# Performance work log

Measured on AMD Instinct MI355X. Metric: run time of the kernel, lower is better.

Reference implementation:

```python
import jax, jax.numpy as jnp
import numpy as np

N = 40000      # nodes
E = 640000     # edges
R = 4          # relations (n_edge_features)
F = 128        # n_node_features
H = 128        # n_hidden
NB = 2         # num_convolution_blocks
G = 64         # graphs in batch
OUT = 10       # n_output
MAXDEG = 10    # PyG MFConv default max_degree


def setup_inputs() -> dict:
    key = jax.random.key(0)
    ks = jax.random.split(key, 20)
    s = 0.05
    return {
        "x": jax.random.normal(ks[0], (N, F), dtype=jnp.float32),
        "edge_index": jax.random.randint(ks[1], (2, E), 0, N, dtype=jnp.int32),
        "edge_attr": jax.random.randint(ks[2], (E,), 0, R, dtype=jnp.int32),
        "batch_idx": jnp.sort(jax.random.randint(ks[3], (N,), 0, G, dtype=jnp.int32)),
        # node embedding Linear(F -> H)
        "W0": jax.random.normal(ks[4], (F, H), dtype=jnp.float32) * s,
        "b0": jnp.zeros((H,), dtype=jnp.float32),
        # per-block RGCNConv params (stacked over blocks)
        "rgcn_Wrel": jax.random.normal(ks[5], (NB, R, H, H), dtype=jnp.float32) * s,
        "rgcn_Wroot": jax.random.normal(ks[6], (NB, H, H), dtype=jnp.float32) * s,
        "rgcn_b": jnp.zeros((NB, H), dtype=jnp.float32),
        # per-block MFConv params: lins_l (bias) and lins_r (no bias), one per degree 0..MAXDEG
        "mf_Wl": jax.random.normal(ks[7], (NB, MAXDEG + 1, H, H), dtype=jnp.float32) * s,
        "mf_bl": jnp.zeros((NB, MAXDEG + 1, H), dtype=jnp.float32),
        "mf_Wr": jax.random.normal(ks[8], (NB, MAXDEG + 1, H, H), dtype=jnp.float32) * s,
        # after-pool MLP
        "W1": jax.random.normal(ks[9], (H, H), dtype=jnp.float32) * s,
        "b1": jnp.zeros((H,), dtype=jnp.float32),
        "W2": jax.random.normal(ks[10], (H, OUT), dtype=jnp.float32) * s,
        "b2": jnp.zeros((OUT,), dtype=jnp.float32),
    }


def _rgcn(h, Wrel, Wroot, b, src, dst, etype):
    # PyG RGCNConv: per-relation mean of neighbor features, then relation GEMM, plus root + bias
    n = h.shape[0]
    idx = dst * R + etype                                   # fused (node, relation) segment id
    msg = h[src]                                            # [E, H] gather
    sums = jax.ops.segment_sum(msg, idx, num_segments=n * R).reshape(n, R, -1)
    cnt = jax.ops.segment_sum(jnp.ones((msg.shape[0],), h.dtype), idx,
                              num_segments=n * R).reshape(n, R, 1)
    mean = jnp.where(cnt > 0, sums / jnp.maximum(cnt, 1.0), 0.0)
    return jnp.einsum('nrh,rho->no', mean, Wrel) + h @ Wroot + b


def _mfconv(h, Wl, bl, Wr, src, dst, deg):
    # PyG MFConv: sum-aggregate neighbors, then degree-specific lin_l(agg) + lin_r(x)
    n = h.shape[0]
    agg = jax.ops.segment_sum(h[src], dst, num_segments=n)  # [N, H]
    out = jnp.zeros((n, Wl.shape[-1]), h.dtype)
    for d in range(MAXDEG + 1):                             # small fixed loop over degree buckets
        m = (deg == d).astype(h.dtype)[:, None]
        out = out + m * (agg @ Wl[d] + bl[d] + h @ Wr[d])
    return out


def reference(x, edge_index, edge_attr, batch_idx,
              W0, b0, rgcn_Wrel, rgcn_Wroot, rgcn_b,
              mf_Wl, mf_bl, mf_Wr, W1, b1, W2, b2):
    src, dst = edge_index[0], edge_index[1]
    etype = edge_attr
    n = x.shape[0]
    # node degree at targets (all relations), clamped to MAXDEG (PyG MFConv)
    deg = jnp.clip(jax.ops.segment_sum(jnp.ones((src.shape[0],), jnp.int32), dst,
                                       num_segments=n), 0, MAXDEG)
    h = x @ W0 + b0
    for blk in range(NB):
        h = jax.nn.relu(h)
        h = _rgcn(h, rgcn_Wrel[blk], rgcn_Wroot[blk], rgcn_b[blk], src, dst, etype)
        h = jax.nn.relu(h)
        h = _mfconv(h, mf_Wl[blk], mf_bl[blk], mf_Wr[blk], src, dst, deg)
    pooled = jax.ops.segment_sum(h, batch_idx, num_segments=G)  # global add pool [G, H]
    out = jax.nn.relu(pooled @ W1 + b1) @ W2 + b2
    return out
```

## Files before the change

### kernel.cpp

```cpp
#include <hip/hip_runtime.h>
#include <hip/hip_bf16.h>

#define N_NODES 40000
#define N_EDGES 640000
#define R_REL 4
#define F_IN 128
#define H_DIM 128
#define NBLK 2
#define G_GRAPHS 64
#define N_OUT 10
#define MAXDEG 10
#define NSCAN_BLK ((N_NODES + 255) / 256)

typedef unsigned short u16;
typedef float f32x4 __attribute__((ext_vector_type(4)));
typedef short bf16x8 __attribute__((ext_vector_type(8)));

__device__ __forceinline__ float relu_f(float x){ return x > 0.f ? x : 0.f; }

__device__ __forceinline__ u16 f2bf(float f){
  union { float f; unsigned int u; } v; v.f = f;
  unsigned int r = v.u + 0x7fffu + ((v.u >> 16) & 1u);
  return (u16)(r >> 16);
}
__device__ __forceinline__ float b2f(u16 u){
  union { unsigned int u; float f; } v; v.u = ((unsigned int)u) << 16; return v.f;
}
__device__ __forceinline__ float blo(unsigned v){ return b2f((u16)v); }
__device__ __forceinline__ float bhi(unsigned v){ return b2f((u16)(v >> 16)); }

__device__ __forceinline__ void gload16(const void* g, void* l){
  __builtin_amdgcn_global_load_lds(
      (const __attribute__((address_space(1))) void*)g,
      (__attribute__((address_space(3))) void*)l, 16, 0, 0);
}

__global__ void k_cnt(const int* __restrict__ dst, const int* __restrict__ et, int* __restrict__ cnt4){
  int e = blockIdx.x * blockDim.x + threadIdx.x;
  if (e >= N_EDGES) return;
  atomicAdd(&cnt4[dst[e] * R_REL + et[e]], 1);
}

__global__ __launch_bounds__(256) void k_scan_a(const int* __restrict__ cnt4, int* __restrict__ deg,
                                                int* __restrict__ row_ptr, int* __restrict__ bsum,
                                                int* __restrict__ bhist){
  __shared__ int s[256];
  __shared__ int lh[16];
  int tid = threadIdx.x;
  int i = blockIdx.x * 256 + tid;
  if (tid < 16) lh[tid] = 0;
  int d = 0;
  if (i < N_NODES){
    int4 c = *(const int4*)(cnt4 + (size_t)i * 4);
    d = c.x + c.y + c.z + c.w;
    deg[i] = d;
  }
  s[tid] = d;
  __syncthreads();
  if (i < N_NODES){
    int dc = d > MAXDEG ? MAXDEG : d;
    atomicAdd(&lh[dc], 1);
  }
  for (int o = 1; o < 256; o <<= 1){
    int t = (tid >= o) ? s[tid - o] : 0;
    __syncthreads();
    s[tid] += t;
    __syncthreads();
  }
  if (i < N_NODES) row_ptr[i] = s[tid] - d;
  if (tid == 255) bsum[blockIdx.x] = s[255];
  if (tid <= MAXDEG) bhist[blockIdx.x * (MAXDEG + 1) + tid] = lh[tid];
}

__global__ __launch_bounds__(256) void k_scan_b(int* __restrict__ bsum, int* __restrict__ bbase){
  __shared__ int s[256];
  int tid = threadIdx.x;
  int v = (tid < NSCAN_BLK) ? bsum[tid] : 0;
  s[tid] = v;
  __syncthreads();
  for (int o = 1; o < 256; o <<= 1){
    int t = (tid >= o) ? s[tid - o] : 0;
    __syncthreads();
    s[tid] += t;
    __syncthreads();
  }
  if (tid < NSCAN_BLK) bbase[tid] = s[tid] - v;
}

__global__ __launch_bounds__(256) void k_scan_c(int* __restrict__ row_ptr, const int* __restrict__ bbase,
                                                const int* __restrict__ cnt4, int* __restrict__ rel_off){
  int i = blockIdx.x * 256 + threadIdx.x;
  if (i < N_NODES){
    int base = row_ptr[i] + bbase[blockIdx.x];
    row_ptr[i] = base;
    int4 c = *(const int4*)(cnt4 + (size_t)i * 4);
    int4 o;
    o.x = base;
    o.y = base + c.x;
    o.z = o.y + c.y;
    o.w = o.z + c.z;
    *(int4*)(rel_off + (size_t)i * 4) = o;
  }
  if (i == 0) row_ptr[N_NODES] = N_EDGES;
}

__global__ void k_csr_fill(const int* __restrict__ src, const int* __restrict__ dst,
                           const int* __restrict__ et, const int* __restrict__ rel_off,
                           int* __restrict__ cursor, int* __restrict__ esrc){
  int e = blockIdx.x * blockDim.x + threadIdx.x;
  if (e >= N_EDGES) return;
  int cell = dst[e] * R_REL + et[e];
  int p = atomicAdd(&cursor[cell], 1);
  esrc[rel_off[cell] + p] = src[e];
}

__global__ __launch_bounds__(64) void k_bscan(const int* __restrict__ bhist, int* __restrict__ pbase,
                                              int* __restrict__ bcount, int* __restrict__ boff){
  __shared__ int cnt_s[MAXDEG + 1];
  __shared__ int off_s[MAXDEG + 1];
  int d = threadIdx.x;
  if (d <= MAXDEG){
    int run = 0;
    for (int b = 0; b < NSCAN_BLK; ++b){
      pbase[b * (MAXDEG + 1) + d] = run;
      run += bhist[b * (MAXDEG + 1) + d];
    }
    cnt_s[d] = run;
    bcount[d] = run;
  }
  __syncthreads();
  if (d == 0){
    int s = 0;
    for (int dd = 0; dd <= MAXDEG; ++dd){ off_s[dd] = s; boff[dd] = s; s += cnt_s[dd]; }
  }
  __syncthreads();
  if (d <= MAXDEG){
    int base = off_s[d];
    for (int b = 0; b < NSCAN_BLK; ++b) pbase[b * (MAXDEG + 1) + d] += base;
  }
}

__global__ __launch_bounds__(256) void k_bfill(const int* __restrict__ deg, const int* __restrict__ pbase,
                                               int* __restrict__ perm){
  __shared__ int lh[MAXDEG + 1];
  int tid = threadIdx.x;
  if (tid <= MAXDEG) lh[tid] = 0;
  __syncthreads();
  int i = blockIdx.x * 256 + tid;
  if (i < N_NODES){
    int d = deg[i]; if (d > MAXDEG) d = MAXDEG;
    int lpos = atomicAdd(&lh[d], 1);
    perm[pbase[blockIdx.x * (MAXDEG + 1) + d] + lpos] = i;
  }
}

__global__ __launch_bounds__(256) void k_cvtW_all(const float* __restrict__ s0, const float* __restrict__ s1,
                                                  const float* __restrict__ s2, const float* __restrict__ s3,
                                                  const float* __restrict__ s4,
                                                  u16* __restrict__ d0, u16* __restrict__ d1,
                                                  u16* __restrict__ d2, u16* __restrict__ d3,
                                                  u16* __restrict__ d4){
  __shared__ float s[32][33];
  int b = blockIdx.x;
  int m = b >> 4, tile = b & 15;
  const float* S; u16* D; int base;
  if (m < 1){ S = s0; D = d0; base = m; }
  else if (m < 9){ S = s1; D = d1; base = m - 1; }
  else if (m < 11){ S = s2; D = d2; base = m - 9; }
  else if (m < 33){ S = s3; D = d3; base = m - 11; }
  else { S = s4; D = d4; base = m - 33; }
  S += (size_t)base * 16384;
  D += (size_t)base * 16384;
  int tr = (tile >> 2) * 32, tc = (tile & 3) * 32;
  int c = threadIdx.x & 31, r0 = threadIdx.x >> 5;
  #pragma unroll
  for (int i = 0; i < 4; ++i){
    int r = r0 + i * 8;
    s[r][c] = S[(size_t)(tr + r) * 128 + tc + c];
  }
  __syncthreads();
  #pragma unroll
  for (int i = 0; i < 4; ++i){
    int r = r0 + i * 8;
    D[(size_t)(tc + r) * 128 + tr + c] = f2bf(s[c][r]);
  }
}

__global__ void k_cvtx(const float* __restrict__ x, u16* __restrict__ xb){
  int t = blockIdx.x * 256 + threadIdx.x;
  if (t >= (N_NODES * H_DIM) / 4) return;
  float4 v = ((const float4*)x)[t];
  uint2 o = make_uint2((unsigned)f2bf(v.x) | ((unsigned)f2bf(v.y) << 16),
                       (unsigned)f2bf(v.z) | ((unsigned)f2bf(v.w) << 16));
  ((uint2*)xb)[t] = o;
}

__global__ __launch_bounds__(256) void k_rgcn_agg(const u16* __restrict__ hb,
                                                  const int* __restrict__ rel_off,
                                                  const int* __restrict__ row_ptr,
                                                  const int* __restrict__ esrc,
                                                  u16* __restrict__ meanb){
  int node = blockIdx.x * 4 + (threadIdx.x >> 6);
  int lane = threadIdx.x & 63;
  int4 ro = *(const int4*)(rel_off + (size_t)node * 4);
  int nend = row_ptr[node + 1];
  int begs[5] = {ro.x, ro.y, ro.z, ro.w, nend};
  #pragma unroll
  for (int r = 0; r < R_REL; ++r){
    int beg = begs[r], end = begs[r + 1];
    float a0 = 0.f, a1 = 0.f;
    int e = beg;
    for (; e + 4 <= end; e += 4){
      int s0 = esrc[e], s1 = esrc[e + 1], s2 = esrc[e + 2], s3 = esrc[e + 3];
      unsigned v0 = *(const unsigned*)(hb + (size_t)s0 * H_DIM + lane * 2);
      unsigned v1 = *(const unsigned*)(hb + (size_t)s1 * H_DIM + lane * 2);
      unsigned v2 = *(const unsigned*)(hb + (size_t)s2 * H_DIM + lane * 2);
      unsigned v3 = *(const unsigned*)(hb + (size_t)s3 * H_DIM + lane * 2);
      a0 += blo(v0) + blo(v1) + blo(v2) + blo(v3);
      a1 += bhi(v0) + bhi(v1) + bhi(v2) + bhi(v3);
    }
    for (; e < end; ++e){
      unsigned v = *(const unsigned*)(hb + (size_t)esrc[e] * H_DIM + lane * 2);
      a0 += blo(v); a1 += bhi(v);
    }
    int c = end - beg;
    float inv = c > 0 ? 1.f / (float)c : 0.f;
    unsigned o = (unsigned)f2bf(a0 * inv) | ((unsigned)f2bf(a1 * inv) << 16);
    *(unsigned*)(meanb + ((size_t)node * R_REL + r) * H_DIM + lane * 2) = o;
  }
}

__global__ __launch_bounds__(256) void k_mf_agg(const u16* __restrict__ hb,
                                                const int* __restrict__ row_ptr,
                                                const int* __restrict__ esrc,
                                                u16* __restrict__ aggb){
  int node = blockIdx.x * 4 + (threadIdx.x >> 6);
  int lane = threadIdx.x & 63;
  int beg = row_ptr[node], end = row_ptr[node + 1];
  float a0 = 0.f, a1 = 0.f;
  int e = beg;
  for (; e + 4 <= end; e += 4){
    int s0 = esrc[e], s1 = esrc[e + 1], s2 = esrc[e + 2], s3 = esrc[e + 3];
    unsigned v0 = *(const unsigned*)(hb + (size_t)s0 * H_DIM + lane * 2);
    unsigned v1 = *(const unsigned*)(hb + (size_t)s1 * H_DIM + lane * 2);
    unsigned v2 = *(const unsigned*)(hb + (size_t)s2 * H_DIM + lane * 2);
    unsigned v3 = *(const unsigned*)(hb + (size_t)s3 * H_DIM + lane * 2);
    a0 += blo(v0) + blo(v1) + blo(v2) + blo(v3);
    a1 += bhi(v0) + bhi(v1) + bhi(v2) + bhi(v3);
  }
  for (; e < end; ++e){
    unsigned v = *(const unsigned*)(hb + (size_t)esrc[e] * H_DIM + lane * 2);
    a0 += blo(v); a1 += bhi(v);
  }
  unsigned o = (unsigned)f2bf(a0) | ((unsigned)f2bf(a1) << 16);
  *(unsigned*)(aggb + (size_t)node * H_DIM + lane * 2) = o;
}


__global__ __launch_bounds__(512) void k_gemm0(const u16* __restrict__ xb, const u16* __restrict__ wt,
                                               const float* __restrict__ bias, u16* __restrict__ hbo){
  __shared__ u16 lds[32][128];
  int tid = threadIdx.x;
  int w = tid >> 6, lane = tid & 63;
  int m0 = blockIdx.x * 32;
  int rg = lane >> 4, cb = (lane & 15) << 4;
  int srow = w * 4 + rg;
  int swcb = cb ^ ((srow & 7) << 4);
  gload16(xb + (size_t)(m0 + srow) * F_IN + (swcb >> 1), &lds[w * 4][0]);
  __syncthreads();

  int arow = lane & 15, kg = lane >> 4;
  int col = w * 16 + arow;
  f32x4 acc[2];
  acc[0] = (f32x4){0.f, 0.f, 0.f, 0.f};
  acc[1] = (f32x4){0.f, 0.f, 0.f, 0.f};
  bf16x8 b[4];
  #pragma unroll
  for (int kk = 0; kk < 4; ++kk)
    b[kk] = *(const bf16x8*)(wt + (size_t)col * F_IN + kk * 32 + kg * 8);
  #pragma unroll
  for (int rt = 0; rt < 2; ++rt){
    int row = rt * 16 + arow;
    const char* base = (const char*)&lds[0][0] + row * 256;
    int sx = (row & 7) << 4;
    #pragma unroll
    for (int kk = 0; kk < 4; ++kk){
      bf16x8 a = *(const bf16x8*)(base + ((kk * 64 + kg * 16) ^ sx));
      acc[rt] = __builtin_amdgcn_mfma_f32_16x16x32_bf16(a, b[kk], acc[rt], 0, 0, 0);
    }
  }
  float bb = bias[col];
  #pragma unroll
  for (int rt = 0; rt < 2; ++rt)
    #pragma unroll
    for (int j = 0; j < 4; ++j){
      int gr = m0 + rt * 16 + kg * 4 + j;
      hbo[(size_t)gr * H_DIM + col] = f2bf(relu_f(acc[rt][j] + bb));
    }
}

__global__ __launch_bounds__(512) void k_rgcn_gemm(const u16* __restrict__ meanb, const u16* __restrict__ hb,
                                                   const u16* __restrict__ wrel, const u16* __restrict__ wroot,
                                                   const float* __restrict__ bias, u16* __restrict__ hbo){
  __shared__ u16 lds[5][32][128];
  int tid = threadIdx.x;
  int w = tid >> 6, lane = tid & 63;
  int m0 = blockIdx.x * 32;
  int rg = lane >> 4, cb = (lane & 15) << 4;
  int srow = w * 4 + rg;
  int swcb = cb ^ ((srow & 7) << 4);
  #pragma unroll
  for (int s = 0; s < 4; ++s)
    gload16(meanb + ((size_t)(m0 + srow) * R_REL + s) * H_DIM + (swcb >> 1), &lds[s][w * 4][0]);
  gload16(hb + (size_t)(m0 + srow) * H_DIM + (swcb >> 1), &lds[4][w * 4][0]);
  __syncthreads();

  int arow = lane & 15, kg = lane >> 4;
  int col = w * 16 + arow;
  f32x4 acc[2];
  acc[0] = (f32x4){0.f, 0.f, 0.f, 0.f};
  acc[1] = (f32x4){0.f, 0.f, 0.f, 0.f};
  #pragma unroll
  for (int s = 0; s < 5; ++s){
    const u16* WT = (s < 4) ? wrel + (size_t)s * 16384 : wroot;
    bf16x8 b[4];
    #pragma unroll
    for (int kk = 0; kk < 4; ++kk)
      b[kk] = *(const bf16x8*)(WT + (size_t)col * H_DIM + kk * 32 + kg * 8);
    #pragma unroll
    for (int rt = 0; rt < 2; ++rt){
      int row = rt * 16 + arow;
      const char* base = (const char*)&lds[s][0][0] + row * 256;
      int sx = (row & 7) << 4;
      #pragma unroll
      for (int kk = 0; kk < 4; ++kk){
        bf16x8 a = *(const bf16x8*)(base + ((kk * 64 + kg * 16) ^ sx));
        acc[rt] = __builtin_amdgcn_mfma_f32_16x16x32_bf16(a, b[kk], acc[rt], 0, 0, 0);
      }
    }
  }
  float bb = bias[col];
  #pragma unroll
  for (int rt = 0; rt < 2; ++rt)
    #pragma unroll
    for (int j = 0; j < 4; ++j){
      int gr = m0 + rt * 16 + kg * 4 + j;
      hbo[(size_t)gr * H_DIM + col] = f2bf(relu_f(acc[rt][j] + bb));
    }
}

template<int FINAL>
__global__ __launch_bounds__(512) void k_mf_gemm(const u16* __restrict__ aggb, const u16* __restrict__ hb,
                                                 const u16* __restrict__ wl, const u16* __restrict__ wr,
                                                 const float* __restrict__ bl,
                                                 const int* __restrict__ bcount, const int* __restrict__ boff,
                                                 const int* __restrict__ perm,
                                                 u16* __restrict__ hbo, float* __restrict__ hf){
  __shared__ u16 lds[2][32][128];
  __shared__ int rows_s[32];
  int t = blockIdx.x;
  int d = -1, tile = 0;
  for (int dd = 0; dd <= MAXDEG; ++dd){
    int nt = (bcount[dd] + 31) >> 5;
    if (t < nt){ d = dd; tile = t; break; }
    t -= nt;
  }
  if (d < 0) return;
  int cnt_d = bcount[d];
  int start = boff[d] + tile * 32;
  int nrows = cnt_d - tile * 32; if (nrows > 32) nrows = 32;

  int tid = threadIdx.x;
  int w = tid >> 6, lane = tid & 63;
  if (tid < 32) rows_s[tid] = (tid < nrows) ? perm[start + tid] : -1;

  int rg = lane >> 4, cb = (lane & 15) << 4;
  int srow = w * 4 + rg;
  int swcb = cb ^ ((srow & 7) << 4);
  int node = perm[start + (srow < nrows ? srow : 0)];
  gload16(aggb + (size_t)node * H_DIM + (swcb >> 1), &lds[0][w * 4][0]);
  gload16(hb   + (size_t)node * H_DIM + (swcb >> 1), &lds[1][w * 4][0]);
  __syncthreads();

  int arow = lane & 15, kg = lane >> 4;
  int col = w * 16 + arow;
  f32x4 acc[2];
  acc[0] = (f32x4){0.f, 0.f, 0.f, 0.f};
  acc[1] = (f32x4){0.f, 0.f, 0.f, 0.f};
  #pragma unroll
  for (int s = 0; s < 2; ++s){
    const u16* WT = (s ? wr : wl) + (size_t)d * 16384;
    bf16x8 b[4];
    #pragma unroll
    for (int kk = 0; kk < 4; ++kk)
      b[kk] = *(const bf16x8*)(WT + (size_t)col * H_DIM + kk * 32 + kg * 8);
    #pragma unroll
    for (int rt = 0; rt < 2; ++rt){
      int row = rt * 16 + arow;
      const char* base = (const char*)&lds[s][0][0] + row * 256;
      int sx = (row & 7) << 4;
      #pragma unroll
      for (int kk = 0; kk < 4; ++kk){
        bf16x8 a = *(const bf16x8*)(base + ((kk * 64 + kg * 16) ^ sx));
        acc[rt] = __builtin_amdgcn_mfma_f32_16x16x32_bf16(a, b[kk], acc[rt], 0, 0, 0);
      }
    }
  }
  float bb = bl[(size_t)d * H_DIM + col];
  #pragma unroll
  for (int rt = 0; rt < 2; ++rt)
    #pragma unroll
    for (int j = 0; j < 4; ++j){
      int gr = rows_s[rt * 16 + kg * 4 + j];
      if (gr >= 0){
        float v = acc[rt][j] + bb;
        if (FINAL) hf[(size_t)gr * H_DIM + col] = v;
        else       hbo[(size_t)gr * H_DIM + col] = f2bf(relu_f(v));
      }
    }
}

__global__ void k_goff(const int* __restrict__ batch, int* __restrict__ goff){
  int n = blockIdx.x * blockDim.x + threadIdx.x;
  if (n >= N_NODES) return;
  int b = batch[n];
  int bp = (n == 0) ? -1 : batch[n - 1];
  for (int g = bp + 1; g <= b; ++g) goff[g] = n;
  if (n == N_NODES - 1){
    for (int g = b + 1; g <= G_GRAPHS; ++g) goff[g] = N_NODES;
  }
}

__global__ __launch_bounds__(256) void k_pool(const float* __restrict__ h, const int* __restrict__ goff,
                                              float* __restrict__ pooled){
  __shared__ float4 sred[8][32];
  int g = blockIdx.x;
  int tid = threadIdx.x;
  int rg = tid >> 5, lane = tid & 31;
  int beg = goff[g], end = goff[g + 1];
  float4 acc = make_float4(0.f, 0.f, 0.f, 0.f);
  for (int n = beg + rg; n < end; n += 8){
    float4 v = ((const float4*)(h + (size_t)n * H_DIM))[lane];
    acc.x += v.x; acc.y += v.y; acc.z += v.z; acc.w += v.w;
  }
  sred[rg][lane] = acc;
  __syncthreads();
  if (tid < 32){
    float4 s = sred[0][tid];
    #pragma unroll
    for (int r = 1; r < 8; ++r){
      float4 v = sred[r][tid];
      s.x += v.x; s.y += v.y; s.z += v.z; s.w += v.w;
    }
    *(float4*)(pooled + (size_t)g * H_DIM + tid * 4) = s;
  }
}

__global__ void k_mlp1(const float* __restrict__ pooled, const float* __restrict__ W1,
                       const float* __restrict__ b1, float* __restrict__ T){
  int t = blockIdx.x * blockDim.x + threadIdx.x;
  if (t >= G_GRAPHS * H_DIM) return;
  int n = t >> 7, j = t & 127;
  float s = b1[j];
  for (int k = 0; k < H_DIM; ++k) s += pooled[n * H_DIM + k] * W1[k * H_DIM + j];
  T[t] = relu_f(s);
}

__global__ void k_mlp2(const float* __restrict__ T, const float* __restrict__ W2,
                       const float* __restrict__ b2, float* __restrict__ out){
  int t = blockIdx.x * blockDim.x + threadIdx.x;
  if (t >= G_GRAPHS * N_OUT) return;
  int n = t / N_OUT, j = t - n * N_OUT;
  float s = b2[j];
  for (int k = 0; k < H_DIM; ++k) s += T[n * H_DIM + k] * W2[k * N_OUT + j];
  out[t] = s;
}

extern "C" void kernel_launch(void* const* d_in, const int* in_sizes, int n_in,
                              void* d_out, int out_size, void* d_ws, size_t ws_size,
                              hipStream_t stream){
  const float* x      = (const float*)d_in[0];
  const int*   ei     = (const int*)d_in[1];
  const int*   ea     = (const int*)d_in[2];
  const int*   batch  = (const int*)d_in[3];
  const float* W0     = (const float*)d_in[4];
  const float* b0     = (const float*)d_in[5];
  const float* rWrel  = (const float*)d_in[6];
  const float* rWroot = (const float*)d_in[7];
  const float* rb     = (const float*)d_in[8];
  const float* mWl    = (const float*)d_in[9];
  const float* mbl    = (const float*)d_in[10];
  const float* mWr    = (const float*)d_in[11];
  const float* W1     = (const float*)d_in[12];
  const float* b1     = (const float*)d_in[13];
  const float* W2     = (const float*)d_in[14];
  const float* b2     = (const float*)d_in[15];
  float* out = (float*)d_out;

  const int* src = ei;
  const int* dst = ei + N_EDGES;

  char* ws = (char*)d_ws;
  size_t off = 0;
  auto alloc = [&](size_t bytes) -> void* {
    void* p = ws + off;
    off += (bytes + 255) & ~(size_t)255;
    return p;
  };
  u16* xb      = (u16*)alloc((size_t)N_NODES * H_DIM * 2);
  u16* hbA     = (u16*)alloc((size_t)N_NODES * H_DIM * 2);
  u16* hbB     = (u16*)alloc((size_t)N_NODES * H_DIM * 2);
  u16* meanb   = (u16*)alloc((size_t)N_NODES * R_REL * H_DIM * 2);
  u16* aggb    = meanb;
  float* hf    = (float*)alloc((size_t)N_NODES * H_DIM * 4);
  u16* wt0     = (u16*)alloc((size_t)1 * 16384 * 2);
  u16* wtRel   = (u16*)alloc((size_t)NBLK * R_REL * 16384 * 2);
  u16* wtRoot  = (u16*)alloc((size_t)NBLK * 16384 * 2);
  u16* wtWl    = (u16*)alloc((size_t)NBLK * (MAXDEG + 1) * 16384 * 2);
  u16* wtWr    = (u16*)alloc((size_t)NBLK * (MAXDEG + 1) * 16384 * 2);
  float* pooled = (float*)alloc((size_t)G_GRAPHS * H_DIM * 4);
  float* T      = (float*)alloc((size_t)G_GRAPHS * H_DIM * 4);
  int* cnt4     = (int*)alloc((size_t)N_NODES * R_REL * 4);
  int* deg      = (int*)alloc((size_t)N_NODES * 4);
  int* row_ptr  = (int*)alloc((size_t)(N_NODES + 1) * 4);
  int* rel_off  = (int*)alloc((size_t)N_NODES * R_REL * 4);
  int* cursor   = (int*)alloc((size_t)N_NODES * R_REL * 4);
  int* esrc     = (int*)alloc((size_t)N_EDGES * 4);
  int* bsum     = (int*)alloc((size_t)NSCAN_BLK * 4);
  int* bbase    = (int*)alloc((size_t)NSCAN_BLK * 4);
  int* bhist    = (int*)alloc((size_t)NSCAN_BLK * (MAXDEG + 1) * 4);
  int* pbase    = (int*)alloc((size_t)NSCAN_BLK * (MAXDEG + 1) * 4);
  int* perm     = (int*)alloc((size_t)N_NODES * 4);
  int* bcount   = (int*)alloc(16 * 4);
  int* boff     = (int*)alloc(16 * 4);
  int* goff     = (int*)alloc((size_t)(G_GRAPHS + 1) * 4);

  hipMemsetAsync(cnt4, 0, (size_t)N_NODES * R_REL * 4, stream);
  hipMemsetAsync(cursor, 0, (size_t)N_NODES * R_REL * 4, stream);

  k_cnt<<<(N_EDGES + 255) / 256, 256, 0, stream>>>(dst, ea, cnt4);
  k_scan_a<<<NSCAN_BLK, 256, 0, stream>>>(cnt4, deg, row_ptr, bsum, bhist);
  k_scan_b<<<1, 256, 0, stream>>>(bsum, bbase);
  k_scan_c<<<NSCAN_BLK, 256, 0, stream>>>(row_ptr, bbase, cnt4, rel_off);
  k_csr_fill<<<(N_EDGES + 255) / 256, 256, 0, stream>>>(src, dst, ea, rel_off, cursor, esrc);
  k_bscan<<<1, 64, 0, stream>>>(bhist, pbase, bcount, boff);
  k_bfill<<<NSCAN_BLK, 256, 0, stream>>>(deg, pbase, perm);
  k_goff<<<(N_NODES + 255) / 256, 256, 0, stream>>>(batch, goff);

  k_cvtW_all<<<55 * 16, 256, 0, stream>>>(W0, rWrel, rWroot, mWl, mWr,
                                          wt0, wtRel, wtRoot, wtWl, wtWr);
  k_cvtx<<<(N_NODES * H_DIM / 4 + 255) / 256, 256, 0, stream>>>(x, xb);

  k_gemm0<<<N_NODES / 32, 512, 0, stream>>>(xb, wt0, b0, hbA);

  u16* hin = hbA;
  u16* hout = hbB;
  for (int blk = 0; blk < NBLK; ++blk){
    k_rgcn_agg<<<N_NODES / 4, 256, 0, stream>>>(hin, rel_off, row_ptr, esrc, meanb);
    k_rgcn_gemm<<<N_NODES / 32, 512, 0, stream>>>(meanb, hin,
        wtRel + (size_t)blk * R_REL * 16384,
        wtRoot + (size_t)blk * 16384,
        rb + (size_t)blk * H_DIM, hout);
    { u16* tmp = hin; hin = hout; hout = tmp; }

    k_mf_agg<<<N_NODES / 4, 256, 0, stream>>>(hin, row_ptr, esrc, aggb);
    const u16* wl_b = wtWl + (size_t)blk * (MAXDEG + 1) * 16384;
    const u16* wr_b = wtWr + (size_t)blk * (MAXDEG + 1) * 16384;
    const float* bl_b = mbl + (size_t)blk * (MAXDEG + 1) * H_DIM;
    int grid_mf = N_NODES / 32 + MAXDEG + 1;
    if (blk == NBLK - 1)
      k_mf_gemm<1><<<grid_mf, 512, 0, stream>>>(aggb, hin, wl_b, wr_b, bl_b,
                                                bcount, boff, perm, hout, hf);
    else
      k_mf_gemm<0><<<grid_mf, 512, 0, stream>>>(aggb, hin, wl_b, wr_b, bl_b,
                                                bcount, boff, perm, hout, hf);
    { u16* tmp = hin; hin = hout; hout = tmp; }
  }

  k_pool<<<G_GRAPHS, 256, 0, stream>>>(hf, goff, pooled);
  k_mlp1<<<(G_GRAPHS * H_DIM + 255) / 256, 256, 0, stream>>>(pooled, W1, b1, T);
  k_mlp2<<<(G_GRAPHS * N_OUT + 255) / 256, 256, 0, stream>>>(T, W2, b2, out);
}
```

Baseline: 400.5 us.

## Fuse neighbor aggregation into RGCN and MFConv GEMM kernels via LDS staging

Removes the separate RGCN and MFConv aggregation kernels. Each GEMM block now gathers and averages or sums its own 32 rows' neighbor features and writes the bf16 results straight into swizzled LDS, so the intermediate meanb/aggb buffers are never written to or read from global memory. CSR fill also seeds the per-cell cursor with the relation offsets in scan_c, which drops a memset and an indirect load. The cost is that gather latency now sits inside the GEMM blocks, each wave serially handles 4 rows, and there are fewer waves in flight than with the 4-nodes-per-256-thread aggregation grids.

```diff
diff --git a/kernel.cpp b/kernel.cpp
--- a/kernel.cpp
+++ b/kernel.cpp
@@ -88,7 +88,8 @@
 }
 
 __global__ __launch_bounds__(256) void k_scan_c(int* __restrict__ row_ptr, const int* __restrict__ bbase,
-                                                const int* __restrict__ cnt4, int* __restrict__ rel_off){
+                                                const int* __restrict__ cnt4, int* __restrict__ rel_off,
+                                                int* __restrict__ cursor){
   int i = blockIdx.x * 256 + threadIdx.x;
   if (i < N_NODES){
     int base = row_ptr[i] + bbase[blockIdx.x];
@@ -100,18 +101,19 @@
     o.z = o.y + c.y;
     o.w = o.z + c.z;
     *(int4*)(rel_off + (size_t)i * 4) = o;
+    *(int4*)(cursor + (size_t)i * 4) = o;
   }
   if (i == 0) row_ptr[N_NODES] = N_EDGES;
 }
 
 __global__ void k_csr_fill(const int* __restrict__ src, const int* __restrict__ dst,
-                           const int* __restrict__ et, const int* __restrict__ rel_off,
+                           const int* __restrict__ et,
                            int* __restrict__ cursor, int* __restrict__ esrc){
   int e = blockIdx.x * blockDim.x + threadIdx.x;
   if (e >= N_EDGES) return;
   int cell = dst[e] * R_REL + et[e];
   int p = atomicAdd(&cursor[cell], 1);
-  esrc[rel_off[cell] + p] = src[e];
+  esrc[p] = src[e];
 }
 
 __global__ __launch_bounds__(64) void k_bscan(const int* __restrict__ bhist, int* __restrict__ pbase,
@@ -195,67 +197,6 @@
   ((uint2*)xb)[t] = o;
 }
 
-__global__ __launch_bounds__(256) void k_rgcn_agg(const u16* __restrict__ hb,
-                                                  const int* __restrict__ rel_off,
-                                                  const int* __restrict__ row_ptr,
-                                                  const int* __restrict__ esrc,
-                                                  u16* __restrict__ meanb){
-  int node = blockIdx.x * 4 + (threadIdx.x >> 6);
-  int lane = threadIdx.x & 63;
-  int4 ro = *(const int4*)(rel_off + (size_t)node * 4);
-  int nend = row_ptr[node + 1];
-  int begs[5] = {ro.x, ro.y, ro.z, ro.w, nend};
-  #pragma unroll
-  for (int r = 0; r < R_REL; ++r){
-    int beg = begs[r], end = begs[r + 1];
-    float a0 = 0.f, a1 = 0.f;
-    int e = beg;
-    for (; e + 4 <= end; e += 4){
-      int s0 = esrc[e], s1 = esrc[e + 1], s2 = esrc[e + 2], s3 = esrc[e + 3];
-      unsigned v0 = *(const unsigned*)(hb + (size_t)s0 * H_DIM + lane * 2);
-      unsigned v1 = *(const unsigned*)(hb + (size_t)s1 * H_DIM + lane * 2);
-      unsigned v2 = *(const unsigned*)(hb + (size_t)s2 * H_DIM + lane * 2);
-      unsigned v3 = *(const unsigned*)(hb + (size_t)s3 * H_DIM + lane * 2);
-      a0 += blo(v0) + blo(v1) + blo(v2) + blo(v3);
-      a1 += bhi(v0) + bhi(v1) + bhi(v2) + bhi(v3);
-    }
-    for (; e < end; ++e){
-      unsigned v = *(const unsigned*)(hb + (size_t)esrc[e] * H_DIM + lane * 2);
-      a0 += blo(v); a1 += bhi(v);
-    }
-    int c = end - beg;
-    float inv = c > 0 ? 1.f / (float)c : 0.f;
-    unsigned o = (unsigned)f2bf(a0 * inv) | ((unsigned)f2bf(a1 * inv) << 16);
-    *(unsigned*)(meanb + ((size_t)node * R_REL + r) * H_DIM + lane * 2) = o;
-  }
-}
-
-__global__ __launch_bounds__(256) void k_mf_agg(const u16* __restrict__ hb,
-                                                const int* __restrict__ row_ptr,
-                                                const int* __restrict__ esrc,
-                                                u16* __restrict__ aggb){
-  int node = blockIdx.x * 4 + (threadIdx.x >> 6);
-  int lane = threadIdx.x & 63;
-  int beg = row_ptr[node], end = row_ptr[node + 1];
-  float a0 = 0.f, a1 = 0.f;
-  int e = beg;
-  for (; e + 4 <= end; e += 4){
-    int s0 = esrc[e], s1 = esrc[e + 1], s2 = esrc[e + 2], s3 = esrc[e + 3];
-    unsigned v0 = *(const unsigned*)(hb + (size_t)s0 * H_DIM + lane * 2);
-    unsigned v1 = *(const unsigned*)(hb + (size_t)s1 * H_DIM + lane * 2);
-    unsigned v2 = *(const unsigned*)(hb + (size_t)s2 * H_DIM + lane * 2);
-    unsigned v3 = *(const unsigned*)(hb + (size_t)s3 * H_DIM + lane * 2);
-    a0 += blo(v0) + blo(v1) + blo(v2) + blo(v3);
-    a1 += bhi(v0) + bhi(v1) + bhi(v2) + bhi(v3);
-  }
-  for (; e < end; ++e){
-    unsigned v = *(const unsigned*)(hb + (size_t)esrc[e] * H_DIM + lane * 2);
-    a0 += blo(v); a1 += bhi(v);
-  }
-  unsigned o = (unsigned)f2bf(a0) | ((unsigned)f2bf(a1) << 16);
-  *(unsigned*)(aggb + (size_t)node * H_DIM + lane * 2) = o;
-}
-
 
 __global__ __launch_bounds__(512) void k_gemm0(const u16* __restrict__ xb, const u16* __restrict__ wt,
                                                const float* __restrict__ bias, u16* __restrict__ hbo){
@@ -299,20 +240,55 @@
     }
 }
 
-__global__ __launch_bounds__(512) void k_rgcn_gemm(const u16* __restrict__ meanb, const u16* __restrict__ hb,
-                                                   const u16* __restrict__ wrel, const u16* __restrict__ wroot,
-                                                   const float* __restrict__ bias, u16* __restrict__ hbo){
+__global__ __launch_bounds__(512) void k_rgcn_fused(const u16* __restrict__ hb,
+                                                    const int* __restrict__ rel_off,
+                                                    const int* __restrict__ row_ptr,
+                                                    const int* __restrict__ esrc,
+                                                    const u16* __restrict__ wrel, const u16* __restrict__ wroot,
+                                                    const float* __restrict__ bias, u16* __restrict__ hbo){
   __shared__ u16 lds[5][32][128];
   int tid = threadIdx.x;
   int w = tid >> 6, lane = tid & 63;
   int m0 = blockIdx.x * 32;
-  int rg = lane >> 4, cb = (lane & 15) << 4;
-  int srow = w * 4 + rg;
-  int swcb = cb ^ ((srow & 7) << 4);
-  #pragma unroll
-  for (int s = 0; s < 4; ++s)
-    gload16(meanb + ((size_t)(m0 + srow) * R_REL + s) * H_DIM + (swcb >> 1), &lds[s][w * 4][0]);
-  gload16(hb + (size_t)(m0 + srow) * H_DIM + (swcb >> 1), &lds[4][w * 4][0]);
+  {
+    int rg = lane >> 4, cb = (lane & 15) << 4;
+    int srow = w * 4 + rg;
+    int swcb = cb ^ ((srow & 7) << 4);
+    gload16(hb + (size_t)(m0 + srow) * H_DIM + (swcb >> 1), &lds[4][w * 4][0]);
+  }
+  #pragma unroll
+  for (int i = 0; i < 4; ++i){
+    int row = w * 4 + i;
+    int node = m0 + row;
+    int4 ro = *(const int4*)(rel_off + (size_t)node * 4);
+    int nend = row_ptr[node + 1];
+    int begs[5] = {ro.x, ro.y, ro.z, ro.w, nend};
+    int sx = (row & 7) << 4;
+    char* ldsb = (char*)&lds[0][0][0];
+    #pragma unroll
+    for (int r = 0; r < R_REL; ++r){
+      int beg = begs[r], end = begs[r + 1];
+      float a0 = 0.f, a1 = 0.f;
+      int e = beg;
+      for (; e + 4 <= end; e += 4){
+        int s0 = esrc[e], s1 = esrc[e + 1], s2 = esrc[e + 2], s3 = esrc[e + 3];
+        unsigned v0 = *(const unsigned*)(hb + (size_t)s0 * H_DIM + lane * 2);
+        unsigned v1 = *(const unsigned*)(hb + (size_t)s1 * H_DIM + lane * 2);
+        unsigned v2 = *(const unsigned*)(hb + (size_t)s2 * H_DIM + lane * 2);
+        unsigned v3 = *(const unsigned*)(hb + (size_t)s3 * H_DIM + lane * 2);
+        a0 += blo(v0) + blo(v1) + blo(v2) + blo(v3);
+        a1 += bhi(v0) + bhi(v1) + bhi(v2) + bhi(v3);
+      }
+      for (; e < end; ++e){
+        unsigned v = *(const unsigned*)(hb + (size_t)esrc[e] * H_DIM + lane * 2);
+        a0 += blo(v); a1 += bhi(v);
+      }
+      int c = end - beg;
+      float inv = c > 0 ? 1.f / (float)c : 0.f;
+      unsigned o = (unsigned)f2bf(a0 * inv) | ((unsigned)f2bf(a1 * inv) << 16);
+      *(unsigned*)(ldsb + (size_t)r * 8192 + row * 256 + ((lane * 4) ^ sx)) = o;
+    }
+  }
   __syncthreads();
 
   int arow = lane & 15, kg = lane >> 4;
@@ -350,12 +326,14 @@
 }
 
 template<int FINAL>
-__global__ __launch_bounds__(512) void k_mf_gemm(const u16* __restrict__ aggb, const u16* __restrict__ hb,
-                                                 const u16* __restrict__ wl, const u16* __restrict__ wr,
-                                                 const float* __restrict__ bl,
-                                                 const int* __restrict__ bcount, const int* __restrict__ boff,
-                                                 const int* __restrict__ perm,
-                                                 u16* __restrict__ hbo, float* __restrict__ hf){
+__global__ __launch_bounds__(512) void k_mf_fused(const u16* __restrict__ hb,
+                                                  const int* __restrict__ row_ptr,
+                                                  const int* __restrict__ esrc,
+                                                  const u16* __restrict__ wl, const u16* __restrict__ wr,
+                                                  const float* __restrict__ bl,
+                                                  const int* __restrict__ bcount, const int* __restrict__ boff,
+                                                  const int* __restrict__ perm,
+                                                  u16* __restrict__ hbo, float* __restrict__ hf){
   __shared__ u16 lds[2][32][128];
   __shared__ int rows_s[32];
   int t = blockIdx.x;
@@ -374,12 +352,39 @@
   int w = tid >> 6, lane = tid & 63;
   if (tid < 32) rows_s[tid] = (tid < nrows) ? perm[start + tid] : -1;
 
-  int rg = lane >> 4, cb = (lane & 15) << 4;
-  int srow = w * 4 + rg;
-  int swcb = cb ^ ((srow & 7) << 4);
-  int node = perm[start + (srow < nrows ? srow : 0)];
-  gload16(aggb + (size_t)node * H_DIM + (swcb >> 1), &lds[0][w * 4][0]);
-  gload16(hb   + (size_t)node * H_DIM + (swcb >> 1), &lds[1][w * 4][0]);
+  {
+    int rg = lane >> 4, cb = (lane & 15) << 4;
+    int srow = w * 4 + rg;
+    int swcb = cb ^ ((srow & 7) << 4);
+    int node = perm[start + (srow < nrows ? srow : 0)];
+    gload16(hb + (size_t)node * H_DIM + (swcb >> 1), &lds[1][w * 4][0]);
+  }
+  #pragma unroll
+  for (int i = 0; i < 4; ++i){
+    int row = w * 4 + i;
+    if (row < nrows){
+      int node = perm[start + row];
+      int beg = row_ptr[node], end = row_ptr[node + 1];
+      float a0 = 0.f, a1 = 0.f;
+      int e = beg;
+      for (; e + 4 <= end; e += 4){
+        int s0 = esrc[e], s1 = esrc[e + 1], s2 = esrc[e + 2], s3 = esrc[e + 3];
+        unsigned v0 = *(const unsigned*)(hb + (size_t)s0 * H_DIM + lane * 2);
+        unsigned v1 = *(const unsigned*)(hb + (size_t)s1 * H_DIM + lane * 2);
+        unsigned v2 = *(const unsigned*)(hb + (size_t)s2 * H_DIM + lane * 2);
+        unsigned v3 = *(const unsigned*)(hb + (size_t)s3 * H_DIM + lane * 2);
+        a0 += blo(v0) + blo(v1) + blo(v2) + blo(v3);
+        a1 += bhi(v0) + bhi(v1) + bhi(v2) + bhi(v3);
+      }
+      for (; e < end; ++e){
+        unsigned v = *(const unsigned*)(hb + (size_t)esrc[e] * H_DIM + lane * 2);
+        a0 += blo(v); a1 += bhi(v);
+      }
+      unsigned o = (unsigned)f2bf(a0) | ((unsigned)f2bf(a1) << 16);
+      int sx = (row & 7) << 4;
+      *(unsigned*)((char*)&lds[0][0][0] + row * 256 + ((lane * 4) ^ sx)) = o;
+    }
+  }
   __syncthreads();
 
   int arow = lane & 15, kg = lane >> 4;
@@ -510,8 +515,6 @@
   u16* xb      = (u16*)alloc((size_t)N_NODES * H_DIM * 2);
   u16* hbA     = (u16*)alloc((size_t)N_NODES * H_DIM * 2);
   u16* hbB     = (u16*)alloc((size_t)N_NODES * H_DIM * 2);
-  u16* meanb   = (u16*)alloc((size_t)N_NODES * R_REL * H_DIM * 2);
-  u16* aggb    = meanb;
   float* hf    = (float*)alloc((size_t)N_NODES * H_DIM * 4);
   u16* wt0     = (u16*)alloc((size_t)1 * 16384 * 2);
   u16* wtRel   = (u16*)alloc((size_t)NBLK * R_REL * 16384 * 2);
@@ -536,13 +539,12 @@
   int* goff     = (int*)alloc((size_t)(G_GRAPHS + 1) * 4);
 
   hipMemsetAsync(cnt4, 0, (size_t)N_NODES * R_REL * 4, stream);
-  hipMemsetAsync(cursor, 0, (size_t)N_NODES * R_REL * 4, stream);
 
   k_cnt<<<(N_EDGES + 255) / 256, 256, 0, stream>>>(dst, ea, cnt4);
   k_scan_a<<<NSCAN_BLK, 256, 0, stream>>>(cnt4, deg, row_ptr, bsum, bhist);
   k_scan_b<<<1, 256, 0, stream>>>(bsum, bbase);
-  k_scan_c<<<NSCAN_BLK, 256, 0, stream>>>(row_ptr, bbase, cnt4, rel_off);
-  k_csr_fill<<<(N_EDGES + 255) / 256, 256, 0, stream>>>(src, dst, ea, rel_off, cursor, esrc);
+  k_scan_c<<<NSCAN_BLK, 256, 0, stream>>>(row_ptr, bbase, cnt4, rel_off, cursor);
+  k_csr_fill<<<(N_EDGES + 255) / 256, 256, 0, stream>>>(src, dst, ea, cursor, esrc);
   k_bscan<<<1, 64, 0, stream>>>(bhist, pbase, bcount, boff);
   k_bfill<<<NSCAN_BLK, 256, 0, stream>>>(deg, pbase, perm);
   k_goff<<<(N_NODES + 255) / 256, 256, 0, stream>>>(batch, goff);
@@ -556,24 +558,22 @@
   u16* hin = hbA;
   u16* hout = hbB;
   for (int blk = 0; blk < NBLK; ++blk){
-    k_rgcn_agg<<<N_NODES / 4, 256, 0, stream>>>(hin, rel_off, row_ptr, esrc, meanb);
-    k_rgcn_gemm<<<N_NODES / 32, 512, 0, stream>>>(meanb, hin,
+    k_rgcn_fused<<<N_NODES / 32, 512, 0, stream>>>(hin, rel_off, row_ptr, esrc,
         wtRel + (size_t)blk * R_REL * 16384,
         wtRoot + (size_t)blk * 16384,
         rb + (size_t)blk * H_DIM, hout);
     { u16* tmp = hin; hin = hout; hout = tmp; }
 
-    k_mf_agg<<<N_NODES / 4, 256, 0, stream>>>(hin, row_ptr, esrc, aggb);
     const u16* wl_b = wtWl + (size_t)blk * (MAXDEG + 1) * 16384;
     const u16* wr_b = wtWr + (size_t)blk * (MAXDEG + 1) * 16384;
     const float* bl_b = mbl + (size_t)blk * (MAXDEG + 1) * H_DIM;
     int grid_mf = N_NODES / 32 + MAXDEG + 1;
     if (blk == NBLK - 1)
-      k_mf_gemm<1><<<grid_mf, 512, 0, stream>>>(aggb, hin, wl_b, wr_b, bl_b,
-                                                bcount, boff, perm, hout, hf);
+      k_mf_fused<1><<<grid_mf, 512, 0, stream>>>(hin, row_ptr, esrc, wl_b, wr_b, bl_b,
+                                                 bcount, boff, perm, hout, hf);
     else
-      k_mf_gemm<0><<<grid_mf, 512, 0, stream>>>(aggb, hin, wl_b, wr_b, bl_b,
-                                                bcount, boff, perm, hout, hf);
+      k_mf_fused<0><<<grid_mf, 512, 0, stream>>>(hin, row_ptr, esrc, wl_b, wr_b, bl_b,
+                                                 bcount, boff, perm, hout, hf);
     { u16* tmp = hin; hin = hout; hout = tmp; }
   }
 
```

Result: slower. 430.3 us (+7.4%).
